# Optimization experiments

Measured on AMD Instinct MI355X. Metric: run time of the kernel, lower is better.

## Reference

```python
import jax, jax.numpy as jnp
import numpy as np

N_NODES = 100000
N_EDGES = 1600000
IN_DIM, HID_DIM, EMB_DIM, OUT_DIM = 128, 64, 64, 40


def glorot(key, shape):
    lim = float(np.sqrt(6.0 / (shape[0] + shape[1])))
    return jax.random.uniform(key, shape, jnp.float32, -lim, lim)


def setup_inputs() -> dict:
    key = jax.random.key(0)
    ks = jax.random.split(key, 8)
    x = jax.random.normal(ks[0], (N_NODES, IN_DIM), jnp.float32)
    edge_index = jax.random.randint(ks[1], (2, N_EDGES), 0, N_NODES, jnp.int64)
    return {
        "x": x,
        "edge_index": edge_index,
        "W1": glorot(ks[2], (IN_DIM, HID_DIM)),
        "b1": jnp.zeros((HID_DIM,), jnp.float32),
        "W2": glorot(ks[3], (HID_DIM, EMB_DIM)),
        "b2": jnp.zeros((EMB_DIM,), jnp.float32),
        "Wl": glorot(ks[4], (EMB_DIM, OUT_DIM)),
        "bl": jnp.zeros((OUT_DIM,), jnp.float32),
    }


def gcn_conv(x, edge_index, W, b, num_nodes):
    # PyG GCNConv: add self-loops, symmetric normalization, transform, scatter-add.
    loop = jnp.arange(num_nodes, dtype=edge_index.dtype)
    src = jnp.concatenate([edge_index[0], loop])  # message sources (row)
    dst = jnp.concatenate([edge_index[1], loop])  # message targets (col)
    h = x @ W  # [N, out]
    deg = jnp.zeros((num_nodes,), h.dtype).at[dst].add(1.0)
    dinv = jnp.where(deg > 0, jax.lax.rsqrt(deg), 0.0)
    norm = dinv[src] * dinv[dst]  # [E+N]
    msgs = h[src] * norm[:, None]  # gather, memory-bound
    out = jax.ops.segment_sum(msgs, dst, num_segments=num_nodes)
    return out + b


def reference(x, edge_index, W1, b1, W2, b2, Wl, bl):
    h = gcn_conv(x, edge_index, W1, b1, N_NODES)
    h = jax.nn.relu(h)
    # dropout is identity in eval mode
    emb = gcn_conv(h, edge_index, W2, b2, N_NODES)
    logits = emb @ Wl + bl
    return jax.nn.log_softmax(logits, axis=-1)
```

## Files before the change

kernel.cpp:

```cpp
#include <hip/hip_runtime.h>
#include <hip/hip_bf16.h>

#define N_NODES 100000
#define N_EDGES 1600000
#define IN_DIM 128
#define HID_DIM 64
#define EMB_DIM 64
#define OUT_DIM 40
#define NTILES 6250
#define NB 391
#define DEPTH 16
#define FTHRESH 12
#define CAP 5120

typedef __attribute__((ext_vector_type(8))) short bf16x8;
typedef __attribute__((ext_vector_type(4))) float f32x4;

__device__ __forceinline__ float bf2f(unsigned short u) {
    unsigned int v = ((unsigned int)u) << 16;
    float f;
    __builtin_memcpy(&f, &v, 4);
    return f;
}
__device__ __forceinline__ unsigned short f2bf(float f) {
    __hip_bfloat16 b = __float2bfloat16(f);
    unsigned short u;
    __builtin_memcpy(&u, &b, 2);
    return u;
}

__device__ __forceinline__ float loadf(const void* p, size_t i, int isbf) {
    return isbf ? bf2f(((const unsigned short*)p)[i]) : ((const float*)p)[i];
}
__device__ __forceinline__ int loadi(const void* p, size_t i, int is64) {
    return is64 ? (int)(((const long long*)p)[i]) : ((const int*)p)[i];
}

__global__ void k_detect(const unsigned int* __restrict__ xb,
                         const unsigned int* __restrict__ eib,
                         int* __restrict__ flags) {
    int tid = threadIdx.x;
    unsigned int u = xb[tid];
    unsigned int lo_exp = (u >> 7) & 0xFF;
    bool bfplaus = (lo_exp >= 100 && lo_exp <= 140) || ((u & 0xFFFFu) == 0u);
    unsigned long long m1 = __ballot(bfplaus);
    unsigned int hi = eib[2 * tid + 1];
    unsigned long long m2 = __ballot(hi == 0u);
    if (tid == 0) {
        flags[0] = (__popcll(m1) >= 48) ? 1 : 0;
        flags[1] = (m2 == 0xFFFFFFFFFFFFFFFFULL) ? 1 : 0;
    }
}

__global__ void k_ginit(int* __restrict__ gcur) {
    int b = blockIdx.x * blockDim.x + threadIdx.x;
    if (b < NB) gcur[b] = b * CAP;
}

__global__ __launch_bounds__(256) void k_bin(const void* __restrict__ ei,
                                             int* __restrict__ gcur,
                                             unsigned int* __restrict__ binned,
                                             const int* __restrict__ flags, int E) {
    __shared__ unsigned int lbuf[NB * DEPTH];
    __shared__ int lcnt[NB];
    int is64 = flags[1];
    int tid = threadIdx.x;
    for (int b = tid; b < NB; b += 256) lcnt[b] = 0;
    __syncthreads();
    int per = (E + gridDim.x - 1) / gridDim.x;
    int e0 = blockIdx.x * per;
    int e1 = min(e0 + per, E);
    for (int base = e0; base < e1; base += 256) {
        int e = base + tid;
        bool act = (e < e1);
        unsigned int val = 0;
        int b = 0, slot = -1;
        if (act) {
            int s = loadi(ei, e, is64);
            int d = loadi(ei, (size_t)N_EDGES + e, is64);
            b = d >> 8;
            val = ((unsigned int)(d & 255) << 24) | (unsigned int)s;
            slot = atomicAdd(&lcnt[b], 1);
            if (slot < DEPTH) lbuf[b * DEPTH + slot] = val;
        }
        __syncthreads();
        if (act && slot >= DEPTH) {
            int p = atomicAdd(&gcur[b], 1);
            if (p < (b + 1) * CAP) binned[p] = val;
        }
        for (int b2 = tid; b2 < NB; b2 += 256) {
            int c = lcnt[b2];
            if (c > DEPTH) c = DEPTH;
            if (c >= FTHRESH) {
                int p = atomicAdd(&gcur[b2], c);
                int lim = (b2 + 1) * CAP;
                for (int j = 0; j < c; ++j) if (p + j < lim) binned[p + j] = lbuf[b2 * DEPTH + j];
                lcnt[b2] = 0;
            }
        }
        __syncthreads();
    }
    for (int b2 = tid; b2 < NB; b2 += 256) {
        int c = lcnt[b2];
        if (c > DEPTH) c = DEPTH;
        if (c > 0) {
            int p = atomicAdd(&gcur[b2], c);
            int lim = (b2 + 1) * CAP;
            for (int j = 0; j < c; ++j) if (p + j < lim) binned[p + j] = lbuf[b2 * DEPTH + j];
        }
    }
}

__global__ void k_bscan(const int* __restrict__ gcur, int* __restrict__ btot,
                        int* __restrict__ rs) {
    __shared__ int sh[512];
    int t = threadIdx.x;
    int v = 0;
    if (t < NB) {
        v = gcur[t] - t * CAP;
        if (v > CAP) v = CAP;
    }
    sh[t] = v;
    __syncthreads();
    for (int o = 1; o < 512; o <<= 1) {
        int u = (t >= o) ? sh[t - o] : 0;
        __syncthreads();
        sh[t] += u;
        __syncthreads();
    }
    if (t < NB) btot[t] = sh[t] - v;
    if (t == NB) rs[N_NODES] = N_EDGES;
}

__global__ __launch_bounds__(256) void k_regroup(const unsigned int* __restrict__ binned,
                                                 const int* __restrict__ btot,
                                                 const int* __restrict__ gcur,
                                                 int* __restrict__ csr_src,
                                                 int* __restrict__ rs,
                                                 float* __restrict__ dinv) {
    __shared__ int lcnt[256];
    __shared__ int lofs[256];
    int b = blockIdx.x, tid = threadIdx.x;
    int n0 = b * 256;
    int nn = min(256, N_NODES - n0);
    lcnt[tid] = 0;
    __syncthreads();
    int src0 = b * CAP;
    int m = gcur[b] - src0;
    if (m > CAP) m = CAP;
    for (int i = tid; i < m; i += 256) {
        atomicAdd(&lcnt[binned[src0 + i] >> 24], 1);
    }
    __syncthreads();
    int c = lcnt[tid];
    lofs[tid] = c;
    __syncthreads();
    for (int o = 1; o < 256; o <<= 1) {
        int u = (tid >= o) ? lofs[tid - o] : 0;
        __syncthreads();
        lofs[tid] += u;
        __syncthreads();
    }
    int base = btot[b];
    int mystart = base + lofs[tid] - c;
    if (tid < nn) {
        rs[n0 + tid] = mystart;
        dinv[n0 + tid] = rsqrtf(1.0f + (float)c);
    }
    __syncthreads();
    lofs[tid] = mystart;
    __syncthreads();
    for (int i = tid; i < m; i += 256) {
        unsigned int v = binned[src0 + i];
        int p = atomicAdd(&lofs[v >> 24], 1);
        csr_src[p] = v & 0xFFFFFF;
    }
}

__global__ __launch_bounds__(256) void k_gemm1(const void* __restrict__ x,
                                               const void* __restrict__ W1,
                                               const float* __restrict__ dinv,
                                               unsigned short* __restrict__ out,
                                               const int* __restrict__ flags, int n) {
    __shared__ unsigned short W1T[64 * 136];
    int isbf = flags[0];
    int tid = threadIdx.x;
    for (int i = tid; i < IN_DIM * HID_DIM; i += 256) {
        int k = i >> 6, nn = i & 63;
        W1T[nn * 136 + k] = isbf ? ((const unsigned short*)W1)[i] : f2bf(((const float*)W1)[i]);
    }
    __syncthreads();
    int lane = tid & 63;
    int lane16 = lane & 15, quad = lane >> 4;
    bf16x8 bfrag[4][4];
#pragma unroll
    for (int ct = 0; ct < 4; ++ct)
#pragma unroll
        for (int kc = 0; kc < 4; ++kc)
            bfrag[ct][kc] = *(const bf16x8*)&W1T[(ct * 16 + lane16) * 136 + kc * 32 + quad * 8];
    int wid = (blockIdx.x * 256 + tid) >> 6;
    int nw = (gridDim.x * 256) >> 6;
    for (int t = wid; t < NTILES; t += nw) {
        int row0 = t * 16;
        bf16x8 afrag[4];
        if (isbf) {
            const unsigned short* xr = (const unsigned short*)x + (size_t)(row0 + lane16) * IN_DIM;
#pragma unroll
            for (int kc = 0; kc < 4; ++kc)
                afrag[kc] = *(const bf16x8*)(xr + kc * 32 + quad * 8);
        } else {
            const float* xr = (const float*)x + (size_t)(row0 + lane16) * IN_DIM;
#pragma unroll
            for (int kc = 0; kc < 4; ++kc) {
                f32x4 p0 = *(const f32x4*)(xr + kc * 32 + quad * 8);
                f32x4 p1 = *(const f32x4*)(xr + kc * 32 + quad * 8 + 4);
                bf16x8 a;
#pragma unroll
                for (int j = 0; j < 4; ++j) {
                    a[j] = (short)f2bf(p0[j]);
                    a[4 + j] = (short)f2bf(p1[j]);
                }
                afrag[kc] = a;
            }
        }
        f32x4 acc[4] = {};
#pragma unroll
        for (int kc = 0; kc < 4; ++kc)
#pragma unroll
            for (int ct = 0; ct < 4; ++ct)
                acc[ct] = __builtin_amdgcn_mfma_f32_16x16x32_bf16(afrag[kc], bfrag[ct][kc], acc[ct], 0, 0, 0);
        float dv[4];
#pragma unroll
        for (int r = 0; r < 4; ++r) dv[r] = dinv[row0 + quad * 4 + r];
#pragma unroll
        for (int ct = 0; ct < 4; ++ct)
#pragma unroll
            for (int r = 0; r < 4; ++r)
                out[(size_t)(row0 + quad * 4 + r) * HID_DIM + ct * 16 + lane16] = f2bf(acc[ct][r] * dv[r]);
    }
}

__global__ __launch_bounds__(256) void k_aggregate(const unsigned short* __restrict__ g,
                                                   const float* __restrict__ dinv,
                                                   const int* __restrict__ rs,
                                                   const int* __restrict__ csr_src,
                                                   float* __restrict__ out, int n) {
    int lane = threadIdx.x & 63;
    int half = lane >> 5;
    int col2 = lane & 31;
    int node = blockIdx.x * 4 + (threadIdx.x >> 6);
    if (node >= n) return;
    int start = rs[node];
    int m_all = rs[node + 1] - start;
    const ushort2* g2 = (const ushort2*)g;
    float ax = 0.0f, ay = 0.0f;
    for (int base = 0; base < m_all; base += 64) {
        int m = min(64, m_all - base);
        int idx = (lane < m) ? csr_src[start + base + lane] : node;
        int nIt = (m + 7) >> 3;
        for (int it = 0; it < nIt; ++it) {
            int j0 = it * 8 + half * 4;
            int i0 = __shfl(idx, j0 + 0);
            int i1 = __shfl(idx, j0 + 1);
            int i2 = __shfl(idx, j0 + 2);
            int i3 = __shfl(idx, j0 + 3);
            ushort2 p0 = g2[(size_t)i0 * 32 + col2];
            ushort2 p1 = g2[(size_t)i1 * 32 + col2];
            ushort2 p2 = g2[(size_t)i2 * 32 + col2];
            ushort2 p3 = g2[(size_t)i3 * 32 + col2];
            if (j0 + 0 < m) { ax += bf2f(p0.x); ay += bf2f(p0.y); }
            if (j0 + 1 < m) { ax += bf2f(p1.x); ay += bf2f(p1.y); }
            if (j0 + 2 < m) { ax += bf2f(p2.x); ay += bf2f(p2.y); }
            if (j0 + 3 < m) { ax += bf2f(p3.x); ay += bf2f(p3.y); }
        }
    }
    ax += __shfl_xor(ax, 32);
    ay += __shfl_xor(ay, 32);
    if (half == 0) {
        float dd = dinv[node];
        ushort2 ps = g2[(size_t)node * 32 + col2];
        float2 r;
        r.x = (ax + bf2f(ps.x)) * dd;
        r.y = (ay + bf2f(ps.y)) * dd;
        ((float2*)out)[(size_t)node * 32 + col2] = r;
    }
}

__global__ __launch_bounds__(256) void k_gemm2(const float* __restrict__ in,
                                               const void* __restrict__ W2,
                                               const void* __restrict__ b1,
                                               const float* __restrict__ dinv,
                                               unsigned short* __restrict__ out,
                                               const int* __restrict__ flags, int n) {
    __shared__ unsigned short W2T[64 * 72];
    __shared__ float bs[64];
    int isbf = flags[0];
    int tid = threadIdx.x;
    for (int i = tid; i < HID_DIM * EMB_DIM; i += 256) {
        int k = i >> 6, nn = i & 63;
        W2T[nn * 72 + k] = isbf ? ((const unsigned short*)W2)[i] : f2bf(((const float*)W2)[i]);
    }
    if (tid < 64) bs[tid] = loadf(b1, tid, isbf);
    __syncthreads();
    int lane = tid & 63;
    int lane16 = lane & 15, quad = lane >> 4;
    bf16x8 bfrag[4][2];
#pragma unroll
    for (int ct = 0; ct < 4; ++ct)
#pragma unroll
        for (int kc = 0; kc < 2; ++kc)
            bfrag[ct][kc] = *(const bf16x8*)&W2T[(ct * 16 + lane16) * 72 + kc * 32 + quad * 8];
    float bv[2][8];
#pragma unroll
    for (int kc = 0; kc < 2; ++kc)
#pragma unroll
        for (int j = 0; j < 8; ++j) bv[kc][j] = bs[kc * 32 + quad * 8 + j];
    int wid = (blockIdx.x * 256 + tid) >> 6;
    int nw = (gridDim.x * 256) >> 6;
    for (int t = wid; t < NTILES; t += nw) {
        int row0 = t * 16;
        const float* ir = in + (size_t)(row0 + lane16) * HID_DIM;
        bf16x8 afrag[2];
#pragma unroll
        for (int kc = 0; kc < 2; ++kc) {
            f32x4 p0 = *(const f32x4*)(ir + kc * 32 + quad * 8);
            f32x4 p1 = *(const f32x4*)(ir + kc * 32 + quad * 8 + 4);
            bf16x8 a;
#pragma unroll
            for (int j = 0; j < 4; ++j) {
                a[j]     = (short)f2bf(fmaxf(p0[j] + bv[kc][j], 0.0f));
                a[4 + j] = (short)f2bf(fmaxf(p1[j] + bv[kc][4 + j], 0.0f));
            }
            afrag[kc] = a;
        }
        f32x4 acc[4] = {};
#pragma unroll
        for (int kc = 0; kc < 2; ++kc)
#pragma unroll
            for (int ct = 0; ct < 4; ++ct)
                acc[ct] = __builtin_amdgcn_mfma_f32_16x16x32_bf16(afrag[kc], bfrag[ct][kc], acc[ct], 0, 0, 0);
        float dv[4];
#pragma unroll
        for (int r = 0; r < 4; ++r) dv[r] = dinv[row0 + quad * 4 + r];
#pragma unroll
        for (int ct = 0; ct < 4; ++ct)
#pragma unroll
            for (int r = 0; r < 4; ++r)
                out[(size_t)(row0 + quad * 4 + r) * EMB_DIM + ct * 16 + lane16] = f2bf(acc[ct][r] * dv[r]);
    }
}

__global__ __launch_bounds__(256) void k_final(const float* __restrict__ in,
                                               const void* __restrict__ b2,
                                               const void* __restrict__ Wl,
                                               const void* __restrict__ bl,
                                               void* __restrict__ out,
                                               const int* __restrict__ flags, int n) {
    __shared__ unsigned short WlT[48 * 72];
    __shared__ float b2s[64];
    int isbf = flags[0];
    int tid = threadIdx.x;
    for (int i = tid; i < 48 * 64; i += 256) {
        int nn = i >> 6, k = i & 63;
        WlT[nn * 72 + k] = (nn < OUT_DIM) ?
            (isbf ? ((const unsigned short*)Wl)[k * OUT_DIM + nn] : f2bf(((const float*)Wl)[k * OUT_DIM + nn]))
            : (unsigned short)0;
    }
    if (tid < 64) b2s[tid] = loadf(b2, tid, isbf);
    __syncthreads();
    int lane = tid & 63;
    int lane16 = lane & 15, quad = lane >> 4;
    bf16x8 bfrag[3][2];
#pragma unroll
    for (int ct = 0; ct < 3; ++ct)
#pragma unroll
        for (int kc = 0; kc < 2; ++kc)
            bfrag[ct][kc] = *(const bf16x8*)&WlT[(ct * 16 + lane16) * 72 + kc * 32 + quad * 8];
    float b2v[2][8];
#pragma unroll
    for (int kc = 0; kc < 2; ++kc)
#pragma unroll
        for (int j = 0; j < 8; ++j) b2v[kc][j] = b2s[kc * 32 + quad * 8 + j];
    float blv[3];
    bool v2 = (lane16 < 8);
#pragma unroll
    for (int ct = 0; ct < 3; ++ct) {
        int col = ct * 16 + lane16;
        blv[ct] = (col < OUT_DIM) ? loadf(bl, col, isbf) : 0.0f;
    }
    int wid = (blockIdx.x * 256 + tid) >> 6;
    int nw = (gridDim.x * 256) >> 6;
    for (int t = wid; t < NTILES; t += nw) {
        int row0 = t * 16;
        const float* ir = in + (size_t)(row0 + lane16) * EMB_DIM;
        bf16x8 afrag[2];
#pragma unroll
        for (int kc = 0; kc < 2; ++kc) {
            f32x4 p0 = *(const f32x4*)(ir + kc * 32 + quad * 8);
            f32x4 p1 = *(const f32x4*)(ir + kc * 32 + quad * 8 + 4);
            bf16x8 a;
#pragma unroll
            for (int j = 0; j < 4; ++j) {
                a[j]     = (short)f2bf(p0[j] + b2v[kc][j]);
                a[4 + j] = (short)f2bf(p1[j] + b2v[kc][4 + j]);
            }
            afrag[kc] = a;
        }
        f32x4 acc[3] = {};
#pragma unroll
        for (int kc = 0; kc < 2; ++kc)
#pragma unroll
            for (int ct = 0; ct < 3; ++ct)
                acc[ct] = __builtin_amdgcn_mfma_f32_16x16x32_bf16(afrag[kc], bfrag[ct][kc], acc[ct], 0, 0, 0);
#pragma unroll
        for (int r = 0; r < 4; ++r) {
            float l0 = acc[0][r] + blv[0];
            float l1 = acc[1][r] + blv[1];
            float l2 = v2 ? (acc[2][r] + blv[2]) : -INFINITY;
            float mx = fmaxf(fmaxf(l0, l1), l2);
#pragma unroll
            for (int s = 1; s < 16; s <<= 1) mx = fmaxf(mx, __shfl_xor(mx, s));
            float sm = expf(l0 - mx) + expf(l1 - mx) + (v2 ? expf(l2 - mx) : 0.0f);
#pragma unroll
            for (int s = 1; s < 16; s <<= 1) sm += __shfl_xor(sm, s);
            float ls = mx + logf(sm);
            int row = row0 + quad * 4 + r;
            size_t o = (size_t)row * OUT_DIM;
            if (isbf) {
                __hip_bfloat16* ob = (__hip_bfloat16*)out;
                ob[o + lane16] = __float2bfloat16(l0 - ls);
                ob[o + 16 + lane16] = __float2bfloat16(l1 - ls);
                if (v2) ob[o + 32 + lane16] = __float2bfloat16(l2 - ls);
            } else {
                float* of = (float*)out;
                of[o + lane16] = l0 - ls;
                of[o + 16 + lane16] = l1 - ls;
                if (v2) of[o + 32 + lane16] = l2 - ls;
            }
        }
    }
}

extern "C" void kernel_launch(void* const* d_in, const int* in_sizes, int n_in,
                              void* d_out, int out_size, void* d_ws, size_t ws_size,
                              hipStream_t stream) {
    const void* x  = d_in[0];
    const void* ei = d_in[1];
    const void* W1 = d_in[2];
    const void* b1 = d_in[3];
    const void* W2 = d_in[4];
    const void* b2 = d_in[5];
    const void* Wl = d_in[6];
    const void* bl = d_in[7];

    float* ws = (float*)d_ws;
    int*   flags   = (int*)ws;
    float* dinv    = ws + 64;
    int*   rs      = (int*)(ws + 100096);
    int*   btot    = (int*)(ws + 200224);
    int*   gcur    = (int*)(ws + 200736);
    int*   csr_src = (int*)(ws + 201248);
    unsigned short* g = (unsigned short*)(ws + 1801248);
    float* bufB    = ws + 5001248;
    unsigned int* binned = (unsigned int*)bufB;

    k_detect<<<1, 64, 0, stream>>>((const unsigned int*)x, (const unsigned int*)ei, flags);

    k_ginit<<<2, 256, 0, stream>>>(gcur);
    k_bin<<<512, 256, 0, stream>>>(ei, gcur, binned, flags, N_EDGES);
    k_bscan<<<1, 512, 0, stream>>>(gcur, btot, rs);
    k_regroup<<<NB, 256, 0, stream>>>(binned, btot, gcur, csr_src, rs, dinv);

    k_gemm1<<<640, 256, 0, stream>>>(x, W1, dinv, g, flags, N_NODES);
    k_aggregate<<<25000, 256, 0, stream>>>(g, dinv, rs, csr_src, bufB, N_NODES);

    k_gemm2<<<640, 256, 0, stream>>>(bufB, W2, b1, dinv, g, flags, N_NODES);
    k_aggregate<<<25000, 256, 0, stream>>>(g, dinv, rs, csr_src, bufB, N_NODES);

    k_final<<<640, 256, 0, stream>>>(bufB, b2, Wl, bl, d_out, flags, N_NODES);
}
```

Before: 296.4 us.

## Store aggregate outputs in bf16, widen gather loads, simplify binning, retune grids

Aggregation now writes bf16 rows instead of fp32, and the downstream GEMM and final kernels read bf16 directly. Each lane now gathers 16 bytes per neighbor with eight neighbors in flight per iteration, replacing 4-byte loads. The binning kernel drops its per-iteration barriers and threshold flushes: it keeps a deeper, padded LDS buffer per bin, sends overflow straight to global memory, and flushes once at the end with wave-parallel writes. Regroup uses 512 threads, GEMM grids are doubled, and the binned scratch is moved to overlap the g buffer. This cuts memory traffic and synchronisation, at the cost of an extra bf16 rounding of intermediate activations and more overflow traffic to global atomics.

Result: no change. 299.4 us (+1.0%).

```diff
diff --git a/kernel.cpp b/kernel.cpp
--- a/kernel.cpp
+++ b/kernel.cpp
@@ -9,15 +9,21 @@
 #define OUT_DIM 40
 #define NTILES 6250
 #define NB 391
-#define DEPTH 16
-#define FTHRESH 12
+#define DEPTH 24
+#define DSTRIDE 25
 #define CAP 5120
 
 typedef __attribute__((ext_vector_type(8))) short bf16x8;
 typedef __attribute__((ext_vector_type(4))) float f32x4;
+typedef __attribute__((ext_vector_type(4))) unsigned int u32x4;
 
 __device__ __forceinline__ float bf2f(unsigned short u) {
     unsigned int v = ((unsigned int)u) << 16;
+    float f;
+    __builtin_memcpy(&f, &v, 4);
+    return f;
+}
+__device__ __forceinline__ float u32f(unsigned int v) {
     float f;
     __builtin_memcpy(&f, &v, 4);
     return f;
@@ -61,8 +67,9 @@
                                              int* __restrict__ gcur,
                                              unsigned int* __restrict__ binned,
                                              const int* __restrict__ flags, int E) {
-    __shared__ unsigned int lbuf[NB * DEPTH];
+    __shared__ unsigned int lbuf[NB * DSTRIDE];
     __shared__ int lcnt[NB];
+    __shared__ int pcur[NB];
     int is64 = flags[1];
     int tid = threadIdx.x;
     for (int b = tid; b < NB; b += 256) lcnt[b] = 0;
@@ -70,43 +77,31 @@
     int per = (E + gridDim.x - 1) / gridDim.x;
     int e0 = blockIdx.x * per;
     int e1 = min(e0 + per, E);
-    for (int base = e0; base < e1; base += 256) {
-        int e = base + tid;
-        bool act = (e < e1);
-        unsigned int val = 0;
-        int b = 0, slot = -1;
-        if (act) {
-            int s = loadi(ei, e, is64);
-            int d = loadi(ei, (size_t)N_EDGES + e, is64);
-            b = d >> 8;
-            val = ((unsigned int)(d & 255) << 24) | (unsigned int)s;
-            slot = atomicAdd(&lcnt[b], 1);
-            if (slot < DEPTH) lbuf[b * DEPTH + slot] = val;
-        }
-        __syncthreads();
-        if (act && slot >= DEPTH) {
+    for (int e = e0 + tid; e < e1; e += 256) {
+        int s = loadi(ei, e, is64);
+        int d = loadi(ei, (size_t)N_EDGES + e, is64);
+        int b = d >> 8;
+        unsigned int val = ((unsigned int)(d & 255) << 24) | (unsigned int)s;
+        int slot = atomicAdd(&lcnt[b], 1);
+        if (slot < DEPTH) {
+            lbuf[b * DSTRIDE + slot] = val;
+        } else {
             int p = atomicAdd(&gcur[b], 1);
             if (p < (b + 1) * CAP) binned[p] = val;
         }
-        for (int b2 = tid; b2 < NB; b2 += 256) {
-            int c = lcnt[b2];
-            if (c > DEPTH) c = DEPTH;
-            if (c >= FTHRESH) {
-                int p = atomicAdd(&gcur[b2], c);
-                int lim = (b2 + 1) * CAP;
-                for (int j = 0; j < c; ++j) if (p + j < lim) binned[p + j] = lbuf[b2 * DEPTH + j];
-                lcnt[b2] = 0;
-            }
-        }
-        __syncthreads();
-    }
-    for (int b2 = tid; b2 < NB; b2 += 256) {
-        int c = lcnt[b2];
-        if (c > DEPTH) c = DEPTH;
-        if (c > 0) {
-            int p = atomicAdd(&gcur[b2], c);
-            int lim = (b2 + 1) * CAP;
-            for (int j = 0; j < c; ++j) if (p + j < lim) binned[p + j] = lbuf[b2 * DEPTH + j];
+    }
+    __syncthreads();
+    for (int b = tid; b < NB; b += 256) {
+        int c = min(lcnt[b], DEPTH);
+        pcur[b] = c ? atomicAdd(&gcur[b], c) : 0;
+    }
+    __syncthreads();
+    int lane = tid & 63, wv = tid >> 6;
+    for (int b = wv; b < NB; b += 4) {
+        int c = min(lcnt[b], DEPTH);
+        if (lane < c) {
+            int p = pcur[b] + lane;
+            if (p < (b + 1) * CAP) binned[p] = lbuf[b * DSTRIDE + lane];
         }
     }
 }
@@ -132,7 +127,7 @@
     if (t == NB) rs[N_NODES] = N_EDGES;
 }
 
-__global__ __launch_bounds__(256) void k_regroup(const unsigned int* __restrict__ binned,
+__global__ __launch_bounds__(512) void k_regroup(const unsigned int* __restrict__ binned,
                                                  const int* __restrict__ btot,
                                                  const int* __restrict__ gcur,
                                                  int* __restrict__ csr_src,
@@ -143,34 +138,35 @@
     int b = blockIdx.x, tid = threadIdx.x;
     int n0 = b * 256;
     int nn = min(256, N_NODES - n0);
-    lcnt[tid] = 0;
+    if (tid < 256) lcnt[tid] = 0;
     __syncthreads();
     int src0 = b * CAP;
     int m = gcur[b] - src0;
     if (m > CAP) m = CAP;
-    for (int i = tid; i < m; i += 256) {
+    for (int i = tid; i < m; i += 512) {
         atomicAdd(&lcnt[binned[src0 + i] >> 24], 1);
     }
     __syncthreads();
-    int c = lcnt[tid];
-    lofs[tid] = c;
+    int c = 0;
+    if (tid < 256) { c = lcnt[tid]; lofs[tid] = c; }
     __syncthreads();
     for (int o = 1; o < 256; o <<= 1) {
-        int u = (tid >= o) ? lofs[tid - o] : 0;
+        int u = (tid < 256 && tid >= o) ? lofs[tid - o] : 0;
         __syncthreads();
-        lofs[tid] += u;
+        if (tid < 256) lofs[tid] += u;
         __syncthreads();
     }
     int base = btot[b];
-    int mystart = base + lofs[tid] - c;
-    if (tid < nn) {
-        rs[n0 + tid] = mystart;
-        dinv[n0 + tid] = rsqrtf(1.0f + (float)c);
-    }
-    __syncthreads();
-    lofs[tid] = mystart;
-    __syncthreads();
-    for (int i = tid; i < m; i += 256) {
+    if (tid < 256) {
+        int mystart = base + lofs[tid] - c;
+        if (tid < nn) {
+            rs[n0 + tid] = mystart;
+            dinv[n0 + tid] = rsqrtf(1.0f + (float)c);
+        }
+        lofs[tid] = mystart;
+    }
+    __syncthreads();
+    for (int i = tid; i < m; i += 512) {
         unsigned int v = binned[src0 + i];
         int p = atomicAdd(&lofs[v >> 24], 1);
         csr_src[p] = v & 0xFFFFFF;
@@ -244,49 +240,52 @@
                                                    const float* __restrict__ dinv,
                                                    const int* __restrict__ rs,
                                                    const int* __restrict__ csr_src,
-                                                   float* __restrict__ out, int n) {
+                                                   unsigned short* __restrict__ out, int n) {
     int lane = threadIdx.x & 63;
-    int half = lane >> 5;
-    int col2 = lane & 31;
+    int grp = lane >> 3;
+    int sub = lane & 7;
     int node = blockIdx.x * 4 + (threadIdx.x >> 6);
     if (node >= n) return;
     int start = rs[node];
     int m_all = rs[node + 1] - start;
-    const ushort2* g2 = (const ushort2*)g;
-    float ax = 0.0f, ay = 0.0f;
+    const u32x4* g4 = (const u32x4*)g;
+    float acc[8] = {0.f, 0.f, 0.f, 0.f, 0.f, 0.f, 0.f, 0.f};
     for (int base = 0; base < m_all; base += 64) {
         int m = min(64, m_all - base);
-        int idx = (lane < m) ? csr_src[start + base + lane] : node;
+        int idx = (lane < m) ? csr_src[start + base + lane] : 0;
         int nIt = (m + 7) >> 3;
         for (int it = 0; it < nIt; ++it) {
-            int j0 = it * 8 + half * 4;
-            int i0 = __shfl(idx, j0 + 0);
-            int i1 = __shfl(idx, j0 + 1);
-            int i2 = __shfl(idx, j0 + 2);
-            int i3 = __shfl(idx, j0 + 3);
-            ushort2 p0 = g2[(size_t)i0 * 32 + col2];
-            ushort2 p1 = g2[(size_t)i1 * 32 + col2];
-            ushort2 p2 = g2[(size_t)i2 * 32 + col2];
-            ushort2 p3 = g2[(size_t)i3 * 32 + col2];
-            if (j0 + 0 < m) { ax += bf2f(p0.x); ay += bf2f(p0.y); }
-            if (j0 + 1 < m) { ax += bf2f(p1.x); ay += bf2f(p1.y); }
-            if (j0 + 2 < m) { ax += bf2f(p2.x); ay += bf2f(p2.y); }
-            if (j0 + 3 < m) { ax += bf2f(p3.x); ay += bf2f(p3.y); }
-        }
-    }
-    ax += __shfl_xor(ax, 32);
-    ay += __shfl_xor(ay, 32);
-    if (half == 0) {
+            int j = it * 8 + grp;
+            int s = __shfl(idx, j);
+            float w = (j < m) ? 1.0f : 0.0f;
+            u32x4 p = g4[(size_t)s * 8 + sub];
+#pragma unroll
+            for (int q = 0; q < 4; ++q) {
+                unsigned int u = p[q];
+                acc[2 * q]     = fmaf(w, u32f(u << 16), acc[2 * q]);
+                acc[2 * q + 1] = fmaf(w, u32f(u & 0xFFFF0000u), acc[2 * q + 1]);
+            }
+        }
+    }
+#pragma unroll
+    for (int off = 8; off <= 32; off <<= 1)
+#pragma unroll
+        for (int q = 0; q < 8; ++q) acc[q] += __shfl_xor(acc[q], off);
+    if (grp == 0) {
+        u32x4 ps = g4[(size_t)node * 8 + sub];
         float dd = dinv[node];
-        ushort2 ps = g2[(size_t)node * 32 + col2];
-        float2 r;
-        r.x = (ax + bf2f(ps.x)) * dd;
-        r.y = (ay + bf2f(ps.y)) * dd;
-        ((float2*)out)[(size_t)node * 32 + col2] = r;
-    }
-}
-
-__global__ __launch_bounds__(256) void k_gemm2(const float* __restrict__ in,
+        u32x4 ov;
+#pragma unroll
+        for (int q = 0; q < 4; ++q) {
+            float lo = (acc[2 * q]     + u32f(ps[q] << 16)) * dd;
+            float hi = (acc[2 * q + 1] + u32f(ps[q] & 0xFFFF0000u)) * dd;
+            ov[q] = (unsigned int)f2bf(lo) | ((unsigned int)f2bf(hi) << 16);
+        }
+        ((u32x4*)out)[(size_t)node * 8 + sub] = ov;
+    }
+}
+
+__global__ __launch_bounds__(256) void k_gemm2(const unsigned short* __restrict__ in,
                                                const void* __restrict__ W2,
                                                const void* __restrict__ b1,
                                                const float* __restrict__ dinv,
@@ -319,17 +318,16 @@
     int nw = (gridDim.x * 256) >> 6;
     for (int t = wid; t < NTILES; t += nw) {
         int row0 = t * 16;
-        const float* ir = in + (size_t)(row0 + lane16) * HID_DIM;
+        const unsigned short* ir = in + (size_t)(row0 + lane16) * HID_DIM;
         bf16x8 afrag[2];
 #pragma unroll
         for (int kc = 0; kc < 2; ++kc) {
-            f32x4 p0 = *(const f32x4*)(ir + kc * 32 + quad * 8);
-            f32x4 p1 = *(const f32x4*)(ir + kc * 32 + quad * 8 + 4);
+            bf16x8 raw = *(const bf16x8*)(ir + kc * 32 + quad * 8);
             bf16x8 a;
 #pragma unroll
-            for (int j = 0; j < 4; ++j) {
-                a[j]     = (short)f2bf(fmaxf(p0[j] + bv[kc][j], 0.0f));
-                a[4 + j] = (short)f2bf(fmaxf(p1[j] + bv[kc][4 + j], 0.0f));
+            for (int j = 0; j < 8; ++j) {
+                float f = fmaxf(bf2f((unsigned short)raw[j]) + bv[kc][j], 0.0f);
+                a[j] = (short)f2bf(f);
             }
             afrag[kc] = a;
         }
@@ -350,7 +348,7 @@
     }
 }
 
-__global__ __launch_bounds__(256) void k_final(const float* __restrict__ in,
+__global__ __launch_bounds__(256) void k_final(const unsigned short* __restrict__ in,
                                                const void* __restrict__ b2,
                                                const void* __restrict__ Wl,
                                                const void* __restrict__ bl,
@@ -392,17 +390,16 @@
     int nw = (gridDim.x * 256) >> 6;
     for (int t = wid; t < NTILES; t += nw) {
         int row0 = t * 16;
-        const float* ir = in + (size_t)(row0 + lane16) * EMB_DIM;
+        const unsigned short* ir = in + (size_t)(row0 + lane16) * EMB_DIM;
         bf16x8 afrag[2];
 #pragma unroll
         for (int kc = 0; kc < 2; ++kc) {
-            f32x4 p0 = *(const f32x4*)(ir + kc * 32 + quad * 8);
-            f32x4 p1 = *(const f32x4*)(ir + kc * 32 + quad * 8 + 4);
+            bf16x8 raw = *(const bf16x8*)(ir + kc * 32 + quad * 8);
             bf16x8 a;
 #pragma unroll
-            for (int j = 0; j < 4; ++j) {
-                a[j]     = (short)f2bf(p0[j] + b2v[kc][j]);
-                a[4 + j] = (short)f2bf(p1[j] + b2v[kc][4 + j]);
+            for (int j = 0; j < 8; ++j) {
+                float f = bf2f((unsigned short)raw[j]) + b2v[kc][j];
+                a[j] = (short)f2bf(f);
             }
             afrag[kc] = a;
         }
@@ -460,22 +457,22 @@
     int*   btot    = (int*)(ws + 200224);
     int*   gcur    = (int*)(ws + 200736);
     int*   csr_src = (int*)(ws + 201248);
-    unsigned short* g = (unsigned short*)(ws + 1801248);
-    float* bufB    = ws + 5001248;
-    unsigned int* binned = (unsigned int*)bufB;
+    unsigned short* g      = (unsigned short*)(ws + 1801248);
+    unsigned short* aggout = (unsigned short*)(ws + 5001248);
+    unsigned int* binned   = (unsigned int*)(ws + 1801248);
 
     k_detect<<<1, 64, 0, stream>>>((const unsigned int*)x, (const unsigned int*)ei, flags);
 
     k_ginit<<<2, 256, 0, stream>>>(gcur);
     k_bin<<<512, 256, 0, stream>>>(ei, gcur, binned, flags, N_EDGES);
     k_bscan<<<1, 512, 0, stream>>>(gcur, btot, rs);
-    k_regroup<<<NB, 256, 0, stream>>>(binned, btot, gcur, csr_src, rs, dinv);
-
-    k_gemm1<<<640, 256, 0, stream>>>(x, W1, dinv, g, flags, N_NODES);
-    k_aggregate<<<25000, 256, 0, stream>>>(g, dinv, rs, csr_src, bufB, N_NODES);
-
-    k_gemm2<<<640, 256, 0, stream>>>(bufB, W2, b1, dinv, g, flags, N_NODES);
-    k_aggregate<<<25000, 256, 0, stream>>>(g, dinv, rs, csr_src, bufB, N_NODES);
-
-    k_final<<<640, 256, 0, stream>>>(bufB, b2, Wl, bl, d_out, flags, N_NODES);
-}
+    k_regroup<<<NB, 512, 0, stream>>>(binned, btot, gcur, csr_src, rs, dinv);
+
+    k_gemm1<<<1280, 256, 0, stream>>>(x, W1, dinv, g, flags, N_NODES);
+    k_aggregate<<<25000, 256, 0, stream>>>(g, dinv, rs, csr_src, aggout, N_NODES);
+
+    k_gemm2<<<1280, 256, 0, stream>>>(aggout, W2, b1, dinv, g, flags, N_NODES);
+    k_aggregate<<<25000, 256, 0, stream>>>(g, dinv, rs, csr_src, aggout, N_NODES);
+
+    k_final<<<1280, 256, 0, stream>>>(aggout, b2, Wl, bl, d_out, flags, N_NODES);
+}
```
